# Kernel tuning notes

Hardware: AMD Instinct MI355X
Metric: run time of the kernel (lower is better)

## Reference

```python
import jax, jax.numpy as jnp
import numpy as np
from jax import lax

B, S, D = 1, 512, 2048
HK, HV, DK, DV, K = 8, 16, 128, 128, 4
R = HV // HK
KEY_DIM = HK * DK
VAL_DIM = HV * DV
CONV_DIM = 2 * KEY_DIM + VAL_DIM
EPS = 1e-6


def setup_inputs() -> dict:
    key = jax.random.key(0)
    ks = jax.random.split(key, 8)
    hidden_states = jax.random.normal(ks[0], (B, S, D), jnp.float32)
    W_qkvz = jax.random.normal(ks[1], (D, 2 * KEY_DIM + 2 * VAL_DIM), jnp.float32) * 0.02
    W_ba = jax.random.normal(ks[2], (D, 2 * HV), jnp.float32) * 0.02
    conv_w = jax.random.normal(ks[3], (CONV_DIM, 1, K), jnp.float32) * 0.2  # depthwise [C,1,K]
    dt_bias = jnp.ones((HV,), jnp.float32)
    A_log = jnp.log(jax.random.uniform(ks[4], (HV,), jnp.float32, 1e-3, 16.0))
    norm_weight = jnp.ones((DV,), jnp.float32)
    W_out = jax.random.normal(ks[5], (VAL_DIM, D), jnp.float32) * 0.02
    return dict(hidden_states=hidden_states, W_qkvz=W_qkvz, W_ba=W_ba, conv_w=conv_w,
                dt_bias=dt_bias, A_log=A_log, norm_weight=norm_weight, W_out=W_out)


def _l2norm(x):
    return x * lax.rsqrt(jnp.sum(x * x, -1, keepdims=True) + EPS)


def reference(hidden_states, W_qkvz, W_ba, conv_w, dt_bias, A_log, norm_weight, W_out):
    # input projections
    qkvz = hidden_states @ W_qkvz              # [B,S,2*key_dim+2*value_dim]
    ba = hidden_states @ W_ba                  # [B,S,2*HV]
    # _rearrange: split per key-head group
    qkvz = qkvz.reshape(B, S, HK, 2 * DK + 2 * R * DV)
    q = qkvz[..., :DK]                                         # [B,S,HK,DK]
    k = qkvz[..., DK:2 * DK]                                   # [B,S,HK,DK]
    v = qkvz[..., 2 * DK:2 * DK + R * DV].reshape(B, S, HV, DV)
    z = qkvz[..., 2 * DK + R * DV:].reshape(B, S, HV, DV)
    ba = ba.reshape(B, S, HK, 2 * R)
    b = ba[..., :R].reshape(B, S, HV)
    a = ba[..., R:].reshape(B, S, HV)
    # fused causal depthwise conv1d + SiLU over concat(q,k,v)
    mixed = jnp.concatenate([q.reshape(B, S, -1), k.reshape(B, S, -1), v.reshape(B, S, -1)], -1)
    mixed = mixed.transpose(0, 2, 1)           # [B,C,S]
    mixed = lax.conv_general_dilated(mixed, conv_w, (1,), [(K - 1, 0)],
                                     feature_group_count=CONV_DIM,
                                     dimension_numbers=('NCH', 'OIH', 'NCH'))
    mixed = jax.nn.silu(mixed).transpose(0, 2, 1)  # [B,S,C]
    q = mixed[..., :KEY_DIM].reshape(B, S, HK, DK)
    k = mixed[..., KEY_DIM:2 * KEY_DIM].reshape(B, S, HK, DK)
    v = mixed[..., 2 * KEY_DIM:].reshape(B, S, HV, DV)
    # gates
    beta = jax.nn.sigmoid(b)                                   # [B,S,HV]
    g = jnp.exp(-jnp.exp(A_log) * jax.nn.softplus(a + dt_bias))  # per-step decay in (0,1)
    q = _l2norm(q) * (DK ** -0.5)
    k = _l2norm(k)
    q = jnp.repeat(q, R, axis=2)               # GQA expand to HV heads
    k = jnp.repeat(k, R, axis=2)
    # gated delta-rule recurrence over sequence (state per batch/head: [DK,DV])
    def step(Sst, inp):
        qt, kt, vt, gt, bt = inp
        Sst = Sst * gt[..., None, None]
        pred = jnp.einsum('bhk,bhkv->bhv', kt, Sst)
        delta = (vt - pred) * bt[..., None]
        Sst = Sst + jnp.einsum('bhk,bhv->bhkv', kt, delta)
        o = jnp.einsum('bhk,bhkv->bhv', qt, Sst)
        return Sst, o
    xs = (q.transpose(1, 0, 2, 3), k.transpose(1, 0, 2, 3), v.transpose(1, 0, 2, 3),
          g.transpose(1, 0, 2), beta.transpose(1, 0, 2))
    S0 = jnp.zeros((B, HV, DK, DV), jnp.float32)
    _, core = lax.scan(step, S0, xs)           # core: [S,B,HV,DV]
    core = core.transpose(1, 0, 2, 3)          # [B,S,HV,DV]
    # gated RMSNorm per value head, gated by silu(z)
    var = jnp.mean(core * core, -1, keepdims=True)
    normed = core * lax.rsqrt(var + EPS) * norm_weight * jax.nn.silu(z)
    return normed.reshape(B, S, VAL_DIM) @ W_out
```

## Files before the change

kernel.cpp:

```cpp
#include <hip/hip_runtime.h>
#include <hip/hip_bf16.h>
#include <math.h>

#define S_  512
#define D_  2048
#define HK_ 8
#define HV_ 16
#define DK_ 128
#define DV_ 128
#define KEY_DIM_ 1024
#define VAL_DIM_ 2048
#define QKVZ_N  6144
#define EPS_ 1e-6f

typedef __attribute__((ext_vector_type(8))) short short8;
typedef __attribute__((ext_vector_type(4))) float f32x4;
typedef unsigned short ushort_t;
typedef unsigned int uint_t;

__device__ __forceinline__ ushort_t f2bf(float x) {
    uint_t u = __float_as_uint(x);
    return (ushort_t)((u + 0x7FFFu + ((u >> 16) & 1u)) >> 16);
}

__device__ __forceinline__ void gl2lds16(const void* g, void* l) {
    __builtin_amdgcn_global_load_lds((const __attribute__((address_space(1))) uint_t*)g,
                                     (__attribute__((address_space(3))) uint_t*)l, 16, 0, 0);
}
__device__ __forceinline__ void gl2lds4(const void* g, void* l) {
    __builtin_amdgcn_global_load_lds((const __attribute__((address_space(1))) uint_t*)g,
                                     (__attribute__((address_space(3))) uint_t*)l, 4, 0, 0);
}

__global__ __launch_bounds__(256) void convert_bf16(const float* __restrict__ X,
                                                    ushort_t* __restrict__ H, int n4) {
    int i = blockIdx.x * blockDim.x + threadIdx.x;
    if (i >= n4) return;
    float4 v = ((const float4*)X)[i];
    ushort4 h;
    h.x = f2bf(v.x); h.y = f2bf(v.y); h.z = f2bf(v.z); h.w = f2bf(v.w);
    ((ushort4*)H)[i] = h;
}

__global__ __launch_bounds__(256) void transpose_convert(const float* __restrict__ W,
                                                         ushort_t* __restrict__ Th,
                                                         int K, int N) {
    __shared__ float tile[64][65];
    const int kb = blockIdx.y * 64, nb = blockIdx.x * 64;
    const int t = threadIdx.x;
#pragma unroll
    for (int i = 0; i < 4; ++i) {
        int r = (t >> 4) + i * 16;
        int c4 = (t & 15) * 4;
        float4 v = *(const float4*)&W[(size_t)(kb + r) * N + nb + c4];
        tile[r][c4 + 0] = v.x; tile[r][c4 + 1] = v.y;
        tile[r][c4 + 2] = v.z; tile[r][c4 + 3] = v.w;
    }
    __syncthreads();
#pragma unroll
    for (int i = 0; i < 4; ++i) {
        int idx = t + 256 * i;
        int n = idx >> 4;
        int k4 = (idx & 15) * 4;
        ushort4 h;
        h.x = f2bf(tile[k4 + 0][n]); h.y = f2bf(tile[k4 + 1][n]);
        h.z = f2bf(tile[k4 + 2][n]); h.w = f2bf(tile[k4 + 3][n]);
        *(ushort4*)&Th[(size_t)(nb + n) * K + kb + k4] = h;
    }
}

template<int BM, int BN, int WR, int WC>
__global__ __launch_bounds__(256) void gemm_bf16(const ushort_t* __restrict__ A,
                                                 const ushort_t* __restrict__ B,
                                                 float* __restrict__ C,
                                                 int M, int N, int K) {
    constexpr int TM = BM / (16 * WR);
    constexpr int TN = BN / (16 * WC);
    constexpr int AI = (BM / 16) * 2;
    constexpr int BI = (BN / 16) * 2;

    __shared__ __align__(16) ushort_t sA[2][2][BM][32];
    __shared__ __align__(16) ushort_t sB[2][2][BN][32];

    const int t = threadIdx.x;
    const int w = t >> 6, lane = t & 63;
    const int wr = w / WC, wc = w % WC;
    const int lm = lane & 15, quad = lane >> 4;
    const int m0 = blockIdx.y * BM, n0 = blockIdx.x * BN;
    const int lrow = lane >> 2;
    const int lch  = (lane & 3) * 8;

    auto stage = [&](int buf, int k0) {
#pragma unroll
        for (int j = w; j < AI; j += 4) {
            int ks = j & 1, r0 = (j >> 1) * 16;
            gl2lds16(&A[(size_t)(m0 + r0 + lrow) * K + k0 + ks * 32 + lch],
                     &sA[buf][ks][r0][0]);
        }
#pragma unroll
        for (int j = w; j < BI; j += 4) {
            int ks = j & 1, r0 = (j >> 1) * 16;
            gl2lds16(&B[(size_t)(n0 + r0 + lrow) * K + k0 + ks * 32 + lch],
                     &sB[buf][ks][r0][0]);
        }
    };

    f32x4 acc[TM][TN] = {};
    stage(0, 0);
    __syncthreads();

    const int NK = K / 64;
    for (int it = 0; it < NK; ++it) {
        int buf = it & 1;
        if (it + 1 < NK) stage(buf ^ 1, (it + 1) * 64);
#pragma unroll
        for (int ks = 0; ks < 2; ++ks) {
            short8 bf[TN];
#pragma unroll
            for (int ni = 0; ni < TN; ++ni)
                bf[ni] = *(const short8*)&sB[buf][ks][wc * (TN * 16) + ni * 16 + lm][quad * 8];
#pragma unroll
            for (int mi = 0; mi < TM; ++mi) {
                short8 af = *(const short8*)&sA[buf][ks][wr * (TM * 16) + mi * 16 + lm][quad * 8];
#pragma unroll
                for (int ni = 0; ni < TN; ++ni)
                    acc[mi][ni] = __builtin_amdgcn_mfma_f32_16x16x32_bf16(af, bf[ni], acc[mi][ni], 0, 0, 0);
            }
        }
        __syncthreads();
    }

#pragma unroll
    for (int mi = 0; mi < TM; ++mi)
#pragma unroll
        for (int ni = 0; ni < TN; ++ni) {
            int row = m0 + wr * TM * 16 + mi * 16 + quad * 4;
            int col = n0 + wc * TN * 16 + ni * 16 + lm;
#pragma unroll
            for (int r = 0; r < 4; ++r)
                C[(size_t)(row + r) * N + col] = acc[mi][ni][r];
        }
}

__global__ __launch_bounds__(256) void ba_kernel(const float* __restrict__ hid,
                                                 const float* __restrict__ Wba,
                                                 float* __restrict__ ba) {
    const int s = blockIdx.x;
    const int j = threadIdx.x & 31;
    const int kg = threadIdx.x >> 5;
    const float* h = hid + (size_t)s * D_;
    float sum = 0.f;
    const int k0 = kg * 256;
#pragma unroll 8
    for (int k = k0; k < k0 + 256; ++k)
        sum = fmaf(h[k], Wba[(size_t)k * 32 + j], sum);
    __shared__ float red[8][32];
    red[kg][j] = sum;
    __syncthreads();
    if (threadIdx.x < 32) {
        float tot = 0.f;
#pragma unroll
        for (int r = 0; r < 8; ++r) tot += red[r][j];
        ba[s * 32 + j] = tot;
    }
}

__global__ __launch_bounds__(128) void conv_kernel(const float* __restrict__ qkvz,
                                                   const float* __restrict__ conv_w,
                                                   float* __restrict__ qc,
                                                   float* __restrict__ kc,
                                                   float* __restrict__ vc) {
    const int s   = blockIdx.x;
    const int grp = blockIdx.y;
    const int d   = threadIdx.x;

    int col, c;
    if (grp < 8) {
        int hk = grp;
        col = hk * 768 + d;
        c   = hk * 128 + d;
    } else if (grp < 16) {
        int hk = grp - 8;
        col = hk * 768 + 128 + d;
        c   = 1024 + (hk * 128 + d);
    } else {
        int hv = grp - 16;
        col = (hv >> 1) * 768 + 256 + (hv & 1) * 128 + d;
        c   = 2048 + (hv * 128 + d);
    }

    const float w0 = conv_w[c * 4 + 0];
    const float w1 = conv_w[c * 4 + 1];
    const float w2 = conv_w[c * 4 + 2];
    const float w3 = conv_w[c * 4 + 3];

    float x = 0.f;
    if (s - 3 >= 0) x += qkvz[(size_t)(s - 3) * QKVZ_N + col] * w0;
    if (s - 2 >= 0) x += qkvz[(size_t)(s - 2) * QKVZ_N + col] * w1;
    if (s - 1 >= 0) x += qkvz[(size_t)(s - 1) * QKVZ_N + col] * w2;
    x += qkvz[(size_t)s * QKVZ_N + col] * w3;

    x = x / (1.f + expf(-x));

    if (grp < 16) {
        float ss = x * x;
#pragma unroll
        for (int m = 1; m < 64; m <<= 1) ss += __shfl_xor(ss, m);
        __shared__ float red[2];
        int wid = threadIdx.x >> 6;
        if ((threadIdx.x & 63) == 0) red[wid] = ss;
        __syncthreads();
        float tot = red[0] + red[1];
        float scale = rsqrtf(tot + EPS_);
        if (grp < 8) {
            x = x * scale * 0.08838834764831845f;
            qc[((size_t)s * HK_ + grp) * DK_ + d] = x;
        } else {
            x = x * scale;
            kc[((size_t)s * HK_ + (grp - 8)) * DK_ + d] = x;
        }
    } else {
        vc[((size_t)s * HV_ + (grp - 16)) * DV_ + d] = x;
    }
}

__global__ __launch_bounds__(256) void gating_kernel(const float* __restrict__ ba,
                                                     const float* __restrict__ A_log,
                                                     const float* __restrict__ dt_bias,
                                                     float* __restrict__ g,
                                                     float* __restrict__ beta) {
    int id = blockIdx.x * blockDim.x + threadIdx.x;
    if (id >= S_ * HV_) return;
    int s  = id >> 4;
    int hv = id & 15;
    int hk = hv >> 1;
    int r  = hv & 1;
    float b = ba[s * 32 + hk * 4 + r];
    float a = ba[s * 32 + hk * 4 + 2 + r];
    beta[id] = 1.f / (1.f + expf(-b));
    float x  = a + dt_bias[hv];
    float sp = (x > 20.f) ? x : log1pf(expf(x));
    g[id] = expf(-expf(A_log[hv]) * sp);
}

template<int CTRL>
__device__ __forceinline__ float dpp_xor(float x) {
    int v = __builtin_amdgcn_update_dpp(0, __float_as_int(x), CTRL, 0xF, 0xF, true);
    return __int_as_float(v);
}
__device__ __forceinline__ float red16(float x) {
    x += dpp_xor<0xB1>(x);
    x += dpp_xor<0x4E>(x);
    x += dpp_xor<0x141>(x);
    x += dpp_xor<0x140>(x);
    return x;
}

__global__ __launch_bounds__(256) void scan_kernel(const float* __restrict__ qc,
                                                   const float* __restrict__ kc,
                                                   const float* __restrict__ vc,
                                                   const float* __restrict__ gb,
                                                   const float* __restrict__ bb,
                                                   float* __restrict__ core) {
    const int h = blockIdx.y, v0 = blockIdx.x * 16;
    const int t = threadIdx.x;
    const int col = t >> 4, sub = t & 15;
    const int lane = t & 63, w = t >> 6;
    const int v = v0 + col, hk = h >> 1;

    __shared__ __align__(16) float skq[2][32][256];
    __shared__ __align__(16) float sv[2][32][16];
    __shared__ __align__(16) float sgb[2][64];

    auto stage = [&](int buf, int c) {
        int t0 = c * 32;
#pragma unroll
        for (int j = 0; j < 8; ++j) {
            int st = w * 8 + j;
            int tt = t0 + st;
            const float* src = (lane < 32)
                ? &kc[((size_t)tt * HK_ + hk) * DK_ + lane * 4]
                : &qc[((size_t)tt * HK_ + hk) * DK_ + (lane - 32) * 4];
            gl2lds16(src, &skq[buf][st][0]);
        }
#pragma unroll
        for (int i = 0; i < 2; ++i) {
            int blk = w * 2 + i;
            int tt = t0 + blk * 4 + (lane >> 4);
            gl2lds4(&vc[((size_t)tt * HV_ + h) * DV_ + v0 + (lane & 15)],
                    &sv[buf][blk * 4][0]);
        }
        if (w == 0) {
            int tt = t0 + (lane & 31);
            const float* src = (lane < 32) ? &gb[(size_t)tt * HV_ + h]
                                           : &bb[(size_t)tt * HV_ + h];
            gl2lds4(src, &sgb[buf][0]);
        }
    };

    float S[8] = {};
    stage(0, 0);
    __syncthreads();

    for (int c = 0; c < 16; ++c) {
        const int buf = c & 1;
        if (c + 1 < 16) stage(buf ^ 1, c + 1);

        float4 kA[3][2], qA[3][2];
        float vr[3], gr[3], br[3];
        auto rd = [&](int slot, int j) {
            kA[slot][0] = *(const float4*)&skq[buf][j][sub * 8];
            kA[slot][1] = *(const float4*)&skq[buf][j][sub * 8 + 4];
            qA[slot][0] = *(const float4*)&skq[buf][j][128 + sub * 8];
            qA[slot][1] = *(const float4*)&skq[buf][j][128 + sub * 8 + 4];
            vr[slot] = sv[buf][j][col];
            gr[slot] = sgb[buf][j];
            br[slot] = sgb[buf][32 + j];
        };
        rd(0, 0); rd(1, 1);
#pragma unroll
        for (int j = 0; j < 32; ++j) {
            const int sl = j % 3;
            if (j + 2 < 32) rd((j + 2) % 3, j + 2);
            const float gg = gr[sl];
            float d0 = fmaf(kA[sl][0].x, S[0], kA[sl][1].x * S[4]);
            float d1 = fmaf(kA[sl][0].y, S[1], kA[sl][1].y * S[5]);
            float d2 = fmaf(kA[sl][0].z, S[2], kA[sl][1].z * S[6]);
            float d3 = fmaf(kA[sl][0].w, S[3], kA[sl][1].w * S[7]);
            float dk = red16((d0 + d1) + (d2 + d3));
            float delta = fmaf(-gg, dk, vr[sl]) * br[sl];
            S[0] = fmaf(kA[sl][0].x, delta, gg * S[0]);
            S[1] = fmaf(kA[sl][0].y, delta, gg * S[1]);
            S[2] = fmaf(kA[sl][0].z, delta, gg * S[2]);
            S[3] = fmaf(kA[sl][0].w, delta, gg * S[3]);
            S[4] = fmaf(kA[sl][1].x, delta, gg * S[4]);
            S[5] = fmaf(kA[sl][1].y, delta, gg * S[5]);
            S[6] = fmaf(kA[sl][1].z, delta, gg * S[6]);
            S[7] = fmaf(kA[sl][1].w, delta, gg * S[7]);
            float o0 = fmaf(qA[sl][0].x, S[0], qA[sl][1].x * S[4]);
            float o1 = fmaf(qA[sl][0].y, S[1], qA[sl][1].y * S[5]);
            float o2 = fmaf(qA[sl][0].z, S[2], qA[sl][1].z * S[6]);
            float o3 = fmaf(qA[sl][0].w, S[3], qA[sl][1].w * S[7]);
            float o = red16((o0 + o1) + (o2 + o3));
            if (sub == 0)
                core[((size_t)(c * 32 + j) * HV_ + h) * DV_ + v] = o;
        }
        __syncthreads();
    }
}

__global__ __launch_bounds__(128) void normgate_kernel(const float* __restrict__ core,
                                                       const float* __restrict__ qkvz,
                                                       const float* __restrict__ nw,
                                                       ushort_t* __restrict__ nh) {
    const int s  = blockIdx.x;
    const int hv = blockIdx.y;
    const int d  = threadIdx.x;

    float x = core[((size_t)s * HV_ + hv) * DV_ + d];
    float ss = x * x;
#pragma unroll
    for (int m = 1; m < 64; m <<= 1) ss += __shfl_xor(ss, m);
    __shared__ float red[2];
    int wid = threadIdx.x >> 6;
    if ((threadIdx.x & 63) == 0) red[wid] = ss;
    __syncthreads();
    float var = (red[0] + red[1]) * (1.f / 128.f);
    float rs  = rsqrtf(var + EPS_);

    float z  = qkvz[(size_t)s * QKVZ_N + (hv >> 1) * 768 + 512 + (hv & 1) * 128 + d];
    float sz = z / (1.f + expf(-z));

    float y = x * rs * nw[d] * sz;
    nh[(size_t)s * VAL_DIM_ + hv * DV_ + d] = f2bf(y);
}

extern "C" void kernel_launch(void* const* d_in, const int* in_sizes, int n_in,
                              void* d_out, int out_size, void* d_ws, size_t ws_size,
                              hipStream_t stream) {
    const float* hidden  = (const float*)d_in[0];
    const float* W_qkvz  = (const float*)d_in[1];
    const float* W_ba    = (const float*)d_in[2];
    const float* conv_w  = (const float*)d_in[3];
    const float* dt_bias = (const float*)d_in[4];
    const float* A_log   = (const float*)d_in[5];
    const float* norm_w  = (const float*)d_in[6];
    const float* W_out   = (const float*)d_in[7];
    float* out = (float*)d_out;

    char* w = (char*)d_ws;
    auto alloc = [&](size_t bytes) { char* p = w; w += (bytes + 255) & ~(size_t)255; return p; };

    float*    qkvz = (float*)alloc((size_t)S_ * QKVZ_N * 4);
    float*    ba   = (float*)alloc((size_t)S_ * 32 * 4);
    float*    qc   = (float*)alloc((size_t)S_ * KEY_DIM_ * 4);
    float*    kc   = (float*)alloc((size_t)S_ * KEY_DIM_ * 4);
    float*    vc   = (float*)alloc((size_t)S_ * VAL_DIM_ * 4);
    float*    gbuf = (float*)alloc((size_t)S_ * HV_ * 4);
    float*    bbuf = (float*)alloc((size_t)S_ * HV_ * 4);
    float*    core = (float*)alloc((size_t)S_ * VAL_DIM_ * 4);
    ushort_t* hidh = (ushort_t*)alloc((size_t)S_ * D_ * 2);
    ushort_t* nrmh = (ushort_t*)alloc((size_t)S_ * VAL_DIM_ * 2);
    ushort_t* Wqh  = (ushort_t*)alloc((size_t)D_ * QKVZ_N * 2);
    ushort_t* Woh  = (ushort_t*)alloc((size_t)VAL_DIM_ * D_ * 2);

    convert_bf16<<<dim3((S_ * D_ / 4 + 255) / 256), 256, 0, stream>>>(hidden, hidh, S_ * D_ / 4);
    transpose_convert<<<dim3(QKVZ_N / 64, D_ / 64), 256, 0, stream>>>(W_qkvz, Wqh, D_, QKVZ_N);
    transpose_convert<<<dim3(D_ / 64, VAL_DIM_ / 64), 256, 0, stream>>>(W_out, Woh, VAL_DIM_, D_);

    gemm_bf16<128, 128, 2, 2><<<dim3(QKVZ_N / 128, S_ / 128), 256, 0, stream>>>(
        hidh, Wqh, qkvz, S_, QKVZ_N, D_);

    ba_kernel<<<dim3(S_), 256, 0, stream>>>(hidden, W_ba, ba);

    conv_kernel<<<dim3(S_, 32), 128, 0, stream>>>(qkvz, conv_w, qc, kc, vc);

    gating_kernel<<<dim3((S_ * HV_ + 255) / 256), 256, 0, stream>>>(ba, A_log, dt_bias, gbuf, bbuf);

    scan_kernel<<<dim3(DV_ / 16, HV_), 256, 0, stream>>>(qc, kc, vc, gbuf, bbuf, core);

    normgate_kernel<<<dim3(S_, HV_), 128, 0, stream>>>(core, qkvz, norm_w, nrmh);

    gemm_bf16<64, 64, 2, 2><<<dim3(D_ / 64, S_ / 64), 256, 0, stream>>>(
        nrmh, Woh, out, S_, D_, VAL_DIM_);
}
```

Measured before the change: 297.5 us.

## Reformulate delta-rule scan with lagged state update and precomputed per-step scalars

Adds a kernel that precomputes per-head, per-step scalars (k_t·k_{t-1}, products of gates, beta) so the scan can apply the state update one step late. The dot product k_t·S and the output reduction no longer wait on the current rank-1 update, which shortens the serial dependency chain. Work is split across 32 lanes per value column with 8 columns per block, giving twice as many blocks, and the QKVZ GEMM tile changes to 64x128. The cost is an extra kernel launch, extra scalar traffic and a reordered floating-point accumulation.

```diff
diff --git a/kernel.cpp b/kernel.cpp
--- a/kernel.cpp
+++ b/kernel.cpp
@@ -248,29 +248,61 @@
     int v = __builtin_amdgcn_update_dpp(0, __float_as_int(x), CTRL, 0xF, 0xF, true);
     return __int_as_float(v);
 }
-__device__ __forceinline__ float red16(float x) {
+__device__ __forceinline__ float red32(float x) {
     x += dpp_xor<0xB1>(x);
     x += dpp_xor<0x4E>(x);
     x += dpp_xor<0x141>(x);
     x += dpp_xor<0x140>(x);
+    x += __int_as_float(__builtin_amdgcn_ds_swizzle(__float_as_int(x), 0x401F));
     return x;
+}
+
+__global__ __launch_bounds__(256) void scal_kernel(const float* __restrict__ kc,
+                                                   const float* __restrict__ gbuf,
+                                                   const float* __restrict__ bbuf,
+                                                   float* __restrict__ scal) {
+    const int t  = blockIdx.x;
+    const int hk = threadIdx.x >> 5;
+    const int s32 = threadIdx.x & 31;
+
+    float c = 0.f;
+    if (t > 0) {
+        float4 kt = *(const float4*)&kc[((size_t)t * HK_ + hk) * DK_ + s32 * 4];
+        float4 kp = *(const float4*)&kc[((size_t)(t - 1) * HK_ + hk) * DK_ + s32 * 4];
+        c = fmaf(kt.x, kp.x, 0.f) + kt.y * kp.y + kt.z * kp.z + kt.w * kp.w;
+    }
+    c = red32(c);
+
+    if (s32 < 2) {
+        int h = hk * 2 + s32;
+        float gt = gbuf[t * HV_ + h];
+        float gp = (t > 0) ? gbuf[(t - 1) * HV_ + h] : 0.f;
+        float bt = bbuf[t * HV_ + h];
+        float4 o;
+        o.x = -gt * c * bt;
+        o.y = gt * gp;
+        o.z = bt;
+        o.w = gt;
+        *(float4*)&scal[((size_t)h * S_ + t) * 4] = o;
+    }
 }
 
 __global__ __launch_bounds__(256) void scan_kernel(const float* __restrict__ qc,
                                                    const float* __restrict__ kc,
                                                    const float* __restrict__ vc,
-                                                   const float* __restrict__ gb,
-                                                   const float* __restrict__ bb,
+                                                   const float* __restrict__ scal,
                                                    float* __restrict__ core) {
-    const int h = blockIdx.y, v0 = blockIdx.x * 16;
+    const int h = blockIdx.y, v0 = blockIdx.x * 8;
     const int t = threadIdx.x;
-    const int col = t >> 4, sub = t & 15;
     const int lane = t & 63, w = t >> 6;
-    const int v = v0 + col, hk = h >> 1;
+    const int sub = lane & 31, cw = lane >> 5;
+    const int vloc = w * 2 + cw;
+    const int v = v0 + vloc;
+    const int hk = h >> 1;
 
     __shared__ __align__(16) float skq[2][32][256];
-    __shared__ __align__(16) float sv[2][32][16];
-    __shared__ __align__(16) float sgb[2][64];
+    __shared__ __align__(16) float sv[2][32][8];
+    __shared__ __align__(16) float ssc[2][32][4];
 
     auto stage = [&](int buf, int c) {
         int t0 = c * 32;
@@ -283,22 +315,24 @@
                 : &qc[((size_t)tt * HK_ + hk) * DK_ + (lane - 32) * 4];
             gl2lds16(src, &skq[buf][st][0]);
         }
-#pragma unroll
-        for (int i = 0; i < 2; ++i) {
-            int blk = w * 2 + i;
-            int tt = t0 + blk * 4 + (lane >> 4);
-            gl2lds4(&vc[((size_t)tt * HV_ + h) * DV_ + v0 + (lane & 15)],
-                    &sv[buf][blk * 4][0]);
+        {
+            int tt = t0 + w * 8 + (lane >> 3);
+            gl2lds4(&vc[((size_t)tt * HV_ + h) * DV_ + v0 + (lane & 7)],
+                    &sv[buf][w * 8][0]);
         }
         if (w == 0) {
-            int tt = t0 + (lane & 31);
-            const float* src = (lane < 32) ? &gb[(size_t)tt * HV_ + h]
-                                           : &bb[(size_t)tt * HV_ + h];
-            gl2lds4(src, &sgb[buf][0]);
+#pragma unroll
+            for (int i = 0; i < 2; ++i)
+                gl2lds4(&scal[((size_t)h * S_ + t0) * 4 + i * 64 + lane],
+                        ((float*)&ssc[buf][0][0]) + i * 64);
         }
     };
 
-    float S[8] = {};
+    float S0 = 0.f, S1 = 0.f, S2 = 0.f, S3 = 0.f;
+    float4 kp = {0.f, 0.f, 0.f, 0.f};
+    float4 qp = {0.f, 0.f, 0.f, 0.f};
+    float D = 0.f, gprev = 0.f;
+
     stage(0, 0);
     __syncthreads();
 
@@ -306,47 +340,54 @@
         const int buf = c & 1;
         if (c + 1 < 16) stage(buf ^ 1, c + 1);
 
-        float4 kA[3][2], qA[3][2];
-        float vr[3], gr[3], br[3];
+        float2 kA[3], kB[3], qA[3], qB[3];
+        float vr[3];
+        float4 sc[3];
         auto rd = [&](int slot, int j) {
-            kA[slot][0] = *(const float4*)&skq[buf][j][sub * 8];
-            kA[slot][1] = *(const float4*)&skq[buf][j][sub * 8 + 4];
-            qA[slot][0] = *(const float4*)&skq[buf][j][128 + sub * 8];
-            qA[slot][1] = *(const float4*)&skq[buf][j][128 + sub * 8 + 4];
-            vr[slot] = sv[buf][j][col];
-            gr[slot] = sgb[buf][j];
-            br[slot] = sgb[buf][32 + j];
+            kA[slot] = *(const float2*)&skq[buf][j][sub * 2];
+            kB[slot] = *(const float2*)&skq[buf][j][64 + sub * 2];
+            qA[slot] = *(const float2*)&skq[buf][j][128 + sub * 2];
+            qB[slot] = *(const float2*)&skq[buf][j][192 + sub * 2];
+            vr[slot] = sv[buf][j][vloc];
+            sc[slot] = *(const float4*)&ssc[buf][j][0];
         };
         rd(0, 0); rd(1, 1);
 #pragma unroll
         for (int j = 0; j < 32; ++j) {
             const int sl = j % 3;
             if (j + 2 < 32) rd((j + 2) % 3, j + 2);
-            const float gg = gr[sl];
-            float d0 = fmaf(kA[sl][0].x, S[0], kA[sl][1].x * S[4]);
-            float d1 = fmaf(kA[sl][0].y, S[1], kA[sl][1].y * S[5]);
-            float d2 = fmaf(kA[sl][0].z, S[2], kA[sl][1].z * S[6]);
-            float d3 = fmaf(kA[sl][0].w, S[3], kA[sl][1].w * S[7]);
-            float dk = red16((d0 + d1) + (d2 + d3));
-            float delta = fmaf(-gg, dk, vr[sl]) * br[sl];
-            S[0] = fmaf(kA[sl][0].x, delta, gg * S[0]);
-            S[1] = fmaf(kA[sl][0].y, delta, gg * S[1]);
-            S[2] = fmaf(kA[sl][0].z, delta, gg * S[2]);
-            S[3] = fmaf(kA[sl][0].w, delta, gg * S[3]);
-            S[4] = fmaf(kA[sl][1].x, delta, gg * S[4]);
-            S[5] = fmaf(kA[sl][1].y, delta, gg * S[5]);
-            S[6] = fmaf(kA[sl][1].z, delta, gg * S[6]);
-            S[7] = fmaf(kA[sl][1].w, delta, gg * S[7]);
-            float o0 = fmaf(qA[sl][0].x, S[0], qA[sl][1].x * S[4]);
-            float o1 = fmaf(qA[sl][0].y, S[1], qA[sl][1].y * S[5]);
-            float o2 = fmaf(qA[sl][0].z, S[2], qA[sl][1].z * S[6]);
-            float o3 = fmaf(qA[sl][0].w, S[3], qA[sl][1].w * S[7]);
-            float o = red16((o0 + o1) + (o2 + o3));
-            if (sub == 0)
-                core[((size_t)(c * 32 + j) * HV_ + h) * DV_ + v] = o;
+            const float4 s4 = sc[sl];
+            float u0 = fmaf(kA[sl].x, S0, kA[sl].y * S1);
+            float u1 = fmaf(kB[sl].x, S2, kB[sl].y * S3);
+            float U = red32(u0 + u1);
+            S0 = fmaf(kp.x, D, gprev * S0);
+            S1 = fmaf(kp.y, D, gprev * S1);
+            S2 = fmaf(kp.z, D, gprev * S2);
+            S3 = fmaf(kp.w, D, gprev * S3);
+            float o0 = fmaf(qp.x, S0, qp.y * S1);
+            float o1 = fmaf(qp.z, S2, qp.w * S3);
+            float om = red32(o0 + o1);
+            int tg = c * 32 + j;
+            if (sub == 0 && tg > 0)
+                core[((size_t)(tg - 1) * HV_ + h) * DV_ + v] = om;
+            float Q = fmaf(-s4.y, U, vr[sl]) * s4.z;
+            D = fmaf(s4.x, D, Q);
+            kp = make_float4(kA[sl].x, kA[sl].y, kB[sl].x, kB[sl].y);
+            qp = make_float4(qA[sl].x, qA[sl].y, qB[sl].x, qB[sl].y);
+            gprev = s4.w;
         }
         __syncthreads();
     }
+
+    S0 = fmaf(kp.x, D, gprev * S0);
+    S1 = fmaf(kp.y, D, gprev * S1);
+    S2 = fmaf(kp.z, D, gprev * S2);
+    S3 = fmaf(kp.w, D, gprev * S3);
+    float o0 = fmaf(qp.x, S0, qp.y * S1);
+    float o1 = fmaf(qp.z, S2, qp.w * S3);
+    float om = red32(o0 + o1);
+    if (sub == 0)
+        core[((size_t)(S_ - 1) * HV_ + h) * DV_ + v] = om;
 }
 
 __global__ __launch_bounds__(128) void normgate_kernel(const float* __restrict__ core,
@@ -398,6 +439,7 @@
     float*    vc   = (float*)alloc((size_t)S_ * VAL_DIM_ * 4);
     float*    gbuf = (float*)alloc((size_t)S_ * HV_ * 4);
     float*    bbuf = (float*)alloc((size_t)S_ * HV_ * 4);
+    float*    scal = (float*)alloc((size_t)HV_ * S_ * 4 * 4);
     float*    core = (float*)alloc((size_t)S_ * VAL_DIM_ * 4);
     ushort_t* hidh = (ushort_t*)alloc((size_t)S_ * D_ * 2);
     ushort_t* nrmh = (ushort_t*)alloc((size_t)S_ * VAL_DIM_ * 2);
@@ -408,7 +450,7 @@
     transpose_convert<<<dim3(QKVZ_N / 64, D_ / 64), 256, 0, stream>>>(W_qkvz, Wqh, D_, QKVZ_N);
     transpose_convert<<<dim3(D_ / 64, VAL_DIM_ / 64), 256, 0, stream>>>(W_out, Woh, VAL_DIM_, D_);
 
-    gemm_bf16<128, 128, 2, 2><<<dim3(QKVZ_N / 128, S_ / 128), 256, 0, stream>>>(
+    gemm_bf16<64, 128, 1, 4><<<dim3(QKVZ_N / 128, S_ / 64), 256, 0, stream>>>(
         hidh, Wqh, qkvz, S_, QKVZ_N, D_);
 
     ba_kernel<<<dim3(S_), 256, 0, stream>>>(hidden, W_ba, ba);
@@ -417,7 +459,9 @@
 
     gating_kernel<<<dim3((S_ * HV_ + 255) / 256), 256, 0, stream>>>(ba, A_log, dt_bias, gbuf, bbuf);
 
-    scan_kernel<<<dim3(DV_ / 16, HV_), 256, 0, stream>>>(qc, kc, vc, gbuf, bbuf, core);
+    scal_kernel<<<dim3(S_), 256, 0, stream>>>(kc, gbuf, bbuf, scal);
+
+    scan_kernel<<<dim3(DV_ / 8, HV_), 256, 0, stream>>>(qc, kc, vc, scal, core);
 
     normgate_kernel<<<dim3(S_, HV_), 128, 0, stream>>>(core, qkvz, norm_w, nrmh);
 
```

Result: no change. 292.2 us (-1.8%).
